# Kernel tuning notes

Hardware: AMD Instinct MI355X
Metric: run time of the kernel (lower is better)

Reference implementation:

```python
import jax, jax.numpy as jnp
import numpy as np


def setup_inputs() -> dict:
    key = jax.random.key(0)
    kq, kk, kv, ki, ks = jax.random.split(key, 5)
    B, H, S, D, VD, T = 2, 8, 2048, 64, 64, 128
    q = jax.random.normal(kq, (B, H, S, D), dtype=jnp.float32)
    k = jax.random.normal(kk, (B, H, S, D), dtype=jnp.float32)
    v = jax.random.normal(kv, (B, H, S, VD), dtype=jnp.float32)
    topk_indices = jax.random.randint(ki, (B, S, T), 0, S, dtype=jnp.int64)
    topk_scores = jax.random.uniform(ks, (B, S, T), dtype=jnp.float32)
    return {"q": q, "k": k, "v": v, "topk_indices": topk_indices,
            "topk_scores": topk_scores}


def reference(q, k, v, topk_indices, topk_scores):
    # q: (B,H,S,D), k: (B,H,S,D), v: (B,H,S,VD), topk_indices: (B,S,T)
    head_dim = q.shape[-1]
    scale = head_dim ** (-0.5)

    # Gather selected K/V per query directly (no O(S^2) expansion).
    # For each batch b: kb (H,S,D), idx (S,T) -> kb[:, idx, :] (H,S,T,D)
    gather = jax.vmap(lambda xb, ib: xb[:, ib, :])
    k_g = gather(k, topk_indices)  # (B,H,S,T,D)
    v_g = gather(v, topk_indices)  # (B,H,S,T,VD)

    # (B,H,S,T) scores
    attn_scores = jnp.einsum('bhsd,bhstd->bhst', q, k_g) * scale
    attn_weights = jax.nn.softmax(attn_scores, axis=-1)

    # reweight by indexer scores (broadcast over heads), then renormalize
    attn_weights = attn_weights * topk_scores[:, None, :, :]
    attn_weights = attn_weights / (attn_weights.sum(axis=-1, keepdims=True) + 1e-12)

    # (B,H,S,VD)
    output = jnp.einsum('bhst,bhstd->bhsd', attn_weights, v_g)
    return output
```

## Files before the change

kernel.cpp:

```cpp
#include <hip/hip_runtime.h>
#include <math.h>


#define BB 2
#define HH 8
#define SS 2048
#define DD 64
#define VDD 64
#define TT 128
#define SCALE 0.125f
#define NKV (BB * HH * SS * DD)

__device__ __forceinline__ float bf_lo(unsigned int u) {
    return __uint_as_float(u << 16);
}
__device__ __forceinline__ float bf_hi(unsigned int u) {
    return __uint_as_float(u);
}
__device__ __forceinline__ unsigned short f2bf_rne(float f) {
    unsigned int u = __float_as_uint(f);
    u += 0x7FFFu + ((u >> 16) & 1u);
    return (unsigned short)(u >> 16);
}

__global__ __launch_bounds__(256) void cvt_kv_bf16(
    const float* __restrict__ k, const float* __restrict__ v,
    unsigned int* __restrict__ kb, unsigned int* __restrict__ vb)
{
    int i = (blockIdx.x * 256 + threadIdx.x) * 4;
    if (i >= NKV) return;
    float4 kf = *(const float4*)(k + i);
    float4 vf = *(const float4*)(v + i);
    unsigned int k0 = (unsigned int)f2bf_rne(kf.x) | ((unsigned int)f2bf_rne(kf.y) << 16);
    unsigned int k1 = (unsigned int)f2bf_rne(kf.z) | ((unsigned int)f2bf_rne(kf.w) << 16);
    unsigned int v0 = (unsigned int)f2bf_rne(vf.x) | ((unsigned int)f2bf_rne(vf.y) << 16);
    unsigned int v1 = (unsigned int)f2bf_rne(vf.z) | ((unsigned int)f2bf_rne(vf.w) << 16);
    *(uint2*)(kb + i / 2) = make_uint2(k0, k1);
    *(uint2*)(vb + i / 2) = make_uint2(v0, v1);
}

__global__ __launch_bounds__(256, 4) void dsa_sparse_attn_bf16(
    const float* __restrict__ q,
    const unsigned int* __restrict__ kb,
    const unsigned int* __restrict__ vb,
    const int* __restrict__ topk_idx,
    const float* __restrict__ topk_sc,
    float* __restrict__ out)
{
    const int tid  = threadIdx.x;
    const int wave = tid >> 6;
    const int lane = tid & 63;
    const int h    = lane & 7;
    const int g    = lane >> 3;

    const int plane = blockIdx.x & 15;
    const int s     = (blockIdx.x >> 4) * 4 + wave;
    const int b     = plane >> 3;

    const float*        qp  = q  + ((size_t)plane * SS + s) * DD;
    const unsigned int* kp  = kb + (size_t)plane * SS * (DD / 2);
    const unsigned int* vp  = vb + (size_t)plane * SS * (VDD / 2);
    const int*          ip  = topk_idx + ((size_t)b * SS + s) * TT;
    const float*        scp = topk_sc  + ((size_t)b * SS + s) * TT;
    float*              op  = out + ((size_t)plane * SS + s) * VDD;

    int   iv0 = ip[lane];
    int   iv1 = ip[64 + lane];
    float sv0 = scp[lane];
    float sv1 = scp[64 + lane];
    float4 qa = *(const float4*)(qp + h * 8);
    float4 qb = *(const float4*)(qp + h * 8 + 4);
    qa.x *= SCALE; qa.y *= SCALE; qa.z *= SCALE; qa.w *= SCALE;
    qb.x *= SCALE; qb.y *= SCALE; qb.z *= SCALE; qb.w *= SCALE;

    float sco[16];
    #pragma unroll
    for (int tc = 0; tc < 8; ++tc) {
        int idx = __shfl(iv0, tc * 8 + g);
        uint4 kk = *(const uint4*)(kp + (size_t)idx * 32 + h * 4);
        float acc;
        acc  = qa.x * bf_lo(kk.x) + qa.y * bf_hi(kk.x);
        acc += qa.z * bf_lo(kk.y) + qa.w * bf_hi(kk.y);
        acc += qb.x * bf_lo(kk.z) + qb.y * bf_hi(kk.z);
        acc += qb.z * bf_lo(kk.w) + qb.w * bf_hi(kk.w);
        acc += __shfl_xor(acc, 1);
        acc += __shfl_xor(acc, 2);
        acc += __shfl_xor(acc, 4);
        sco[tc] = acc;
    }
    #pragma unroll
    for (int tc = 0; tc < 8; ++tc) {
        int idx = __shfl(iv1, tc * 8 + g);
        uint4 kk = *(const uint4*)(kp + (size_t)idx * 32 + h * 4);
        float acc;
        acc  = qa.x * bf_lo(kk.x) + qa.y * bf_hi(kk.x);
        acc += qa.z * bf_lo(kk.y) + qa.w * bf_hi(kk.y);
        acc += qb.x * bf_lo(kk.z) + qb.y * bf_hi(kk.z);
        acc += qb.z * bf_lo(kk.w) + qb.w * bf_hi(kk.w);
        acc += __shfl_xor(acc, 1);
        acc += __shfl_xor(acc, 2);
        acc += __shfl_xor(acc, 4);
        sco[8 + tc] = acc;
    }

    float m = sco[0];
    #pragma unroll
    for (int tc = 1; tc < 16; ++tc) m = fmaxf(m, sco[tc]);
    m = fmaxf(m, __shfl_xor(m, 8));
    m = fmaxf(m, __shfl_xor(m, 16));
    m = fmaxf(m, __shfl_xor(m, 32));
    float sum = 0.f;
    #pragma unroll
    for (int tc = 0; tc < 8; ++tc) {
        float e = __expf(sco[tc] - m) * __shfl(sv0, tc * 8 + g);
        sco[tc] = e;
        sum += e;
    }
    #pragma unroll
    for (int tc = 0; tc < 8; ++tc) {
        float e = __expf(sco[8 + tc] - m) * __shfl(sv1, tc * 8 + g);
        sco[8 + tc] = e;
        sum += e;
    }
    sum += __shfl_xor(sum, 8);
    sum += __shfl_xor(sum, 16);
    sum += __shfl_xor(sum, 32);
    float inv = 1.0f / (sum + 1e-12f);

    float a[8] = {0.f, 0.f, 0.f, 0.f, 0.f, 0.f, 0.f, 0.f};
    #pragma unroll
    for (int tc = 0; tc < 8; ++tc) {
        int   idx = __shfl(iv0, tc * 8 + g);
        float w   = sco[tc] * inv;
        uint4 u = *(const uint4*)(vp + (size_t)idx * 32 + h * 4);
        a[0] = fmaf(w, bf_lo(u.x), a[0]);  a[1] = fmaf(w, bf_hi(u.x), a[1]);
        a[2] = fmaf(w, bf_lo(u.y), a[2]);  a[3] = fmaf(w, bf_hi(u.y), a[3]);
        a[4] = fmaf(w, bf_lo(u.z), a[4]);  a[5] = fmaf(w, bf_hi(u.z), a[5]);
        a[6] = fmaf(w, bf_lo(u.w), a[6]);  a[7] = fmaf(w, bf_hi(u.w), a[7]);
    }
    #pragma unroll
    for (int tc = 0; tc < 8; ++tc) {
        int   idx = __shfl(iv1, tc * 8 + g);
        float w   = sco[8 + tc] * inv;
        uint4 u = *(const uint4*)(vp + (size_t)idx * 32 + h * 4);
        a[0] = fmaf(w, bf_lo(u.x), a[0]);  a[1] = fmaf(w, bf_hi(u.x), a[1]);
        a[2] = fmaf(w, bf_lo(u.y), a[2]);  a[3] = fmaf(w, bf_hi(u.y), a[3]);
        a[4] = fmaf(w, bf_lo(u.z), a[4]);  a[5] = fmaf(w, bf_hi(u.z), a[5]);
        a[6] = fmaf(w, bf_lo(u.w), a[6]);  a[7] = fmaf(w, bf_hi(u.w), a[7]);
    }
    #pragma unroll
    for (int j = 0; j < 8; ++j) {
        a[j] += __shfl_xor(a[j], 8);
        a[j] += __shfl_xor(a[j], 16);
        a[j] += __shfl_xor(a[j], 32);
    }
    if (g == 0) {
        *(float4*)(op + h * 8)     = make_float4(a[0], a[1], a[2], a[3]);
        *(float4*)(op + h * 8 + 4) = make_float4(a[4], a[5], a[6], a[7]);
    }
}

__global__ __launch_bounds__(256, 4) void dsa_sparse_attn_f32(
    const float* __restrict__ q,
    const float* __restrict__ k,
    const float* __restrict__ v,
    const int* __restrict__ topk_idx,
    const float* __restrict__ topk_sc,
    float* __restrict__ out)
{
    const int tid  = threadIdx.x;
    const int wave = tid >> 6;
    const int lane = tid & 63;
    const int plane = blockIdx.x & 15;
    const int s     = (blockIdx.x >> 4) * 4 + wave;
    const int b     = plane >> 3;

    const float* qp  = q + ((size_t)plane * SS + s) * DD;
    const float* kp  = k + (size_t)plane * SS * DD;
    const float* vp  = v + (size_t)plane * SS * VDD;
    const int*   ip  = topk_idx + ((size_t)b * SS + s) * TT;
    const float* scp = topk_sc  + ((size_t)b * SS + s) * TT;
    float*       op  = out + ((size_t)plane * SS + s) * VDD;

    __shared__ int   s_idx[4][TT];
    __shared__ float s_w[4][TT];

    float sc0 = scp[lane];
    float sc1 = scp[64 + lane];
    s_idx[wave][lane]      = ip[lane];
    s_idx[wave][64 + lane] = ip[64 + lane];

    const int l = lane & 3;
    const int g = lane >> 2;
    float4 qf[4];
    #pragma unroll
    for (int j = 0; j < 4; ++j) qf[j] = *(const float4*)(qp + l * 4 + 16 * j);
    __syncthreads();

    #pragma unroll
    for (int tc = 0; tc < 8; ++tc) {
        int t = tc * 16 + g;
        const float* krow = kp + (size_t)s_idx[wave][t] * DD;
        float acc = 0.f;
        #pragma unroll
        for (int j = 0; j < 4; ++j) {
            float4 kf = *(const float4*)(krow + l * 4 + 16 * j);
            acc += qf[j].x * kf.x + qf[j].y * kf.y + qf[j].z * kf.z + qf[j].w * kf.w;
        }
        acc += __shfl_xor(acc, 1);
        acc += __shfl_xor(acc, 2);
        if (l == 0) s_w[wave][t] = acc * SCALE;
    }
    __syncthreads();

    float a0 = s_w[wave][lane];
    float a1 = s_w[wave][64 + lane];
    float m = fmaxf(a0, a1);
    #pragma unroll
    for (int off = 32; off >= 1; off >>= 1) m = fmaxf(m, __shfl_xor(m, off));
    float e0 = __expf(a0 - m) * sc0;
    float e1 = __expf(a1 - m) * sc1;
    float sum = e0 + e1;
    #pragma unroll
    for (int off = 32; off >= 1; off >>= 1) sum += __shfl_xor(sum, off);
    float inv = 1.0f / (sum + 1e-12f);
    s_w[wave][lane]      = e0 * inv;
    s_w[wave][64 + lane] = e1 * inv;
    __syncthreads();

    float acc = 0.f;
    #pragma unroll 8
    for (int t = 0; t < TT; ++t)
        acc = fmaf(s_w[wave][t], vp[(size_t)s_idx[wave][t] * VDD + lane], acc);
    op[lane] = acc;
}

extern "C" void kernel_launch(void* const* d_in, const int* in_sizes, int n_in,
                              void* d_out, int out_size, void* d_ws, size_t ws_size,
                              hipStream_t stream) {
    const float* q   = (const float*)d_in[0];
    const float* k   = (const float*)d_in[1];
    const float* v   = (const float*)d_in[2];
    const int*   idx = (const int*)d_in[3];
    const float* sc  = (const float*)d_in[4];
    float*       out = (float*)d_out;

    const size_t need = (size_t)NKV * 2 * 2;
    if (ws_size >= need) {
        unsigned int* kb = (unsigned int*)d_ws;
        unsigned int* vb = kb + NKV / 2;
        hipLaunchKernelGGL(cvt_kv_bf16, dim3(NKV / 4 / 256), dim3(256), 0, stream,
                           k, v, kb, vb);
        hipLaunchKernelGGL(dsa_sparse_attn_bf16, dim3(8192), dim3(256), 0, stream,
                           q, kb, vb, idx, sc, out);
    } else {
        hipLaunchKernelGGL(dsa_sparse_attn_f32, dim3(8192), dim3(256), 0, stream,
                           q, k, v, idx, sc, out);
    }
}
```

Baseline: 127.1 us.

## Store K as fp16 with dot2 scoring and fuse softmax with V accumulation

K is converted to fp16 (round-toward-zero packing) instead of bf16, so the QK dot products use packed fdot2 instructions rather than unpacking and scalar FMAs. The softmax exponentiation is merged with the V gather/accumulate loop, and normalization is deferred to a single multiply at output time, which removes the second pass over the scores. V accumulation uses 2-wide packed FMAs. This lowers ALU instruction count, but fp16 K has a narrower range and truncating rounding, which changes accuracy.

```diff
diff --git a/kernel.cpp b/kernel.cpp
--- a/kernel.cpp
+++ b/kernel.cpp
@@ -11,6 +11,9 @@
 #define SCALE 0.125f
 #define NKV (BB * HH * SS * DD)
 
+typedef __fp16 h2 __attribute__((ext_vector_type(2)));
+typedef float  f2 __attribute__((ext_vector_type(2)));
+
 __device__ __forceinline__ float bf_lo(unsigned int u) {
     return __uint_as_float(u << 16);
 }
@@ -22,26 +25,34 @@
     u += 0x7FFFu + ((u >> 16) & 1u);
     return (unsigned short)(u >> 16);
 }
-
-__global__ __launch_bounds__(256) void cvt_kv_bf16(
+__device__ __forceinline__ unsigned int pk_f16(float x, float y) {
+    h2 p = __builtin_amdgcn_cvt_pkrtz(x, y);
+    return __builtin_bit_cast(unsigned int, p);
+}
+__device__ __forceinline__ float dot2(unsigned int qh, unsigned int kh, float c) {
+    return __builtin_amdgcn_fdot2(__builtin_bit_cast(h2, qh),
+                                  __builtin_bit_cast(h2, kh), c, false);
+}
+
+__global__ __launch_bounds__(256) void cvt_kv(
     const float* __restrict__ k, const float* __restrict__ v,
-    unsigned int* __restrict__ kb, unsigned int* __restrict__ vb)
+    unsigned int* __restrict__ kh, unsigned int* __restrict__ vb)
 {
     int i = (blockIdx.x * 256 + threadIdx.x) * 4;
     if (i >= NKV) return;
     float4 kf = *(const float4*)(k + i);
     float4 vf = *(const float4*)(v + i);
-    unsigned int k0 = (unsigned int)f2bf_rne(kf.x) | ((unsigned int)f2bf_rne(kf.y) << 16);
-    unsigned int k1 = (unsigned int)f2bf_rne(kf.z) | ((unsigned int)f2bf_rne(kf.w) << 16);
+    unsigned int k0 = pk_f16(kf.x, kf.y);
+    unsigned int k1 = pk_f16(kf.z, kf.w);
     unsigned int v0 = (unsigned int)f2bf_rne(vf.x) | ((unsigned int)f2bf_rne(vf.y) << 16);
     unsigned int v1 = (unsigned int)f2bf_rne(vf.z) | ((unsigned int)f2bf_rne(vf.w) << 16);
-    *(uint2*)(kb + i / 2) = make_uint2(k0, k1);
+    *(uint2*)(kh + i / 2) = make_uint2(k0, k1);
     *(uint2*)(vb + i / 2) = make_uint2(v0, v1);
 }
 
 __global__ __launch_bounds__(256, 4) void dsa_sparse_attn_bf16(
     const float* __restrict__ q,
-    const unsigned int* __restrict__ kb,
+    const unsigned int* __restrict__ kh,
     const unsigned int* __restrict__ vb,
     const int* __restrict__ topk_idx,
     const float* __restrict__ topk_sc,
@@ -58,7 +69,7 @@
     const int b     = plane >> 3;
 
     const float*        qp  = q  + ((size_t)plane * SS + s) * DD;
-    const unsigned int* kp  = kb + (size_t)plane * SS * (DD / 2);
+    const unsigned int* kp  = kh + (size_t)plane * SS * (DD / 2);
     const unsigned int* vp  = vb + (size_t)plane * SS * (VDD / 2);
     const int*          ip  = topk_idx + ((size_t)b * SS + s) * TT;
     const float*        scp = topk_sc  + ((size_t)b * SS + s) * TT;
@@ -70,19 +81,17 @@
     float sv1 = scp[64 + lane];
     float4 qa = *(const float4*)(qp + h * 8);
     float4 qb = *(const float4*)(qp + h * 8 + 4);
-    qa.x *= SCALE; qa.y *= SCALE; qa.z *= SCALE; qa.w *= SCALE;
-    qb.x *= SCALE; qb.y *= SCALE; qb.z *= SCALE; qb.w *= SCALE;
+    unsigned int q0 = pk_f16(qa.x * SCALE, qa.y * SCALE);
+    unsigned int q1 = pk_f16(qa.z * SCALE, qa.w * SCALE);
+    unsigned int q2 = pk_f16(qb.x * SCALE, qb.y * SCALE);
+    unsigned int q3 = pk_f16(qb.z * SCALE, qb.w * SCALE);
 
     float sco[16];
     #pragma unroll
     for (int tc = 0; tc < 8; ++tc) {
         int idx = __shfl(iv0, tc * 8 + g);
         uint4 kk = *(const uint4*)(kp + (size_t)idx * 32 + h * 4);
-        float acc;
-        acc  = qa.x * bf_lo(kk.x) + qa.y * bf_hi(kk.x);
-        acc += qa.z * bf_lo(kk.y) + qa.w * bf_hi(kk.y);
-        acc += qb.x * bf_lo(kk.z) + qb.y * bf_hi(kk.z);
-        acc += qb.z * bf_lo(kk.w) + qb.w * bf_hi(kk.w);
+        float acc = dot2(q0, kk.x, dot2(q1, kk.y, dot2(q2, kk.z, dot2(q3, kk.w, 0.f))));
         acc += __shfl_xor(acc, 1);
         acc += __shfl_xor(acc, 2);
         acc += __shfl_xor(acc, 4);
@@ -92,11 +101,7 @@
     for (int tc = 0; tc < 8; ++tc) {
         int idx = __shfl(iv1, tc * 8 + g);
         uint4 kk = *(const uint4*)(kp + (size_t)idx * 32 + h * 4);
-        float acc;
-        acc  = qa.x * bf_lo(kk.x) + qa.y * bf_hi(kk.x);
-        acc += qa.z * bf_lo(kk.y) + qa.w * bf_hi(kk.y);
-        acc += qb.x * bf_lo(kk.z) + qb.y * bf_hi(kk.z);
-        acc += qb.z * bf_lo(kk.w) + qb.w * bf_hi(kk.w);
+        float acc = dot2(q0, kk.x, dot2(q1, kk.y, dot2(q2, kk.z, dot2(q3, kk.w, 0.f))));
         acc += __shfl_xor(acc, 1);
         acc += __shfl_xor(acc, 2);
         acc += __shfl_xor(acc, 4);
@@ -109,45 +114,47 @@
     m = fmaxf(m, __shfl_xor(m, 8));
     m = fmaxf(m, __shfl_xor(m, 16));
     m = fmaxf(m, __shfl_xor(m, 32));
+
+    f2 a0 = {0.f, 0.f}, a1 = {0.f, 0.f}, a2 = {0.f, 0.f}, a3 = {0.f, 0.f};
     float sum = 0.f;
     #pragma unroll
     for (int tc = 0; tc < 8; ++tc) {
-        float e = __expf(sco[tc] - m) * __shfl(sv0, tc * 8 + g);
-        sco[tc] = e;
+        int   idx = __shfl(iv0, tc * 8 + g);
+        uint4 u   = *(const uint4*)(vp + (size_t)idx * 32 + h * 4);
+        float e   = __expf(sco[tc] - m) * __shfl(sv0, tc * 8 + g);
         sum += e;
-    }
-    #pragma unroll
-    for (int tc = 0; tc < 8; ++tc) {
-        float e = __expf(sco[8 + tc] - m) * __shfl(sv1, tc * 8 + g);
-        sco[8 + tc] = e;
+        f2 wv = {e, e};
+        f2 vx = {bf_lo(u.x), bf_hi(u.x)};
+        f2 vy = {bf_lo(u.y), bf_hi(u.y)};
+        f2 vz = {bf_lo(u.z), bf_hi(u.z)};
+        f2 vw = {bf_lo(u.w), bf_hi(u.w)};
+        a0 = __builtin_elementwise_fma(wv, vx, a0);
+        a1 = __builtin_elementwise_fma(wv, vy, a1);
+        a2 = __builtin_elementwise_fma(wv, vz, a2);
+        a3 = __builtin_elementwise_fma(wv, vw, a3);
+    }
+    #pragma unroll
+    for (int tc = 0; tc < 8; ++tc) {
+        int   idx = __shfl(iv1, tc * 8 + g);
+        uint4 u   = *(const uint4*)(vp + (size_t)idx * 32 + h * 4);
+        float e   = __expf(sco[8 + tc] - m) * __shfl(sv1, tc * 8 + g);
         sum += e;
-    }
+        f2 wv = {e, e};
+        f2 vx = {bf_lo(u.x), bf_hi(u.x)};
+        f2 vy = {bf_lo(u.y), bf_hi(u.y)};
+        f2 vz = {bf_lo(u.z), bf_hi(u.z)};
+        f2 vw = {bf_lo(u.w), bf_hi(u.w)};
+        a0 = __builtin_elementwise_fma(wv, vx, a0);
+        a1 = __builtin_elementwise_fma(wv, vy, a1);
+        a2 = __builtin_elementwise_fma(wv, vz, a2);
+        a3 = __builtin_elementwise_fma(wv, vw, a3);
+    }
+
     sum += __shfl_xor(sum, 8);
     sum += __shfl_xor(sum, 16);
     sum += __shfl_xor(sum, 32);
-    float inv = 1.0f / (sum + 1e-12f);
-
-    float a[8] = {0.f, 0.f, 0.f, 0.f, 0.f, 0.f, 0.f, 0.f};
-    #pragma unroll
-    for (int tc = 0; tc < 8; ++tc) {
-        int   idx = __shfl(iv0, tc * 8 + g);
-        float w   = sco[tc] * inv;
-        uint4 u = *(const uint4*)(vp + (size_t)idx * 32 + h * 4);
-        a[0] = fmaf(w, bf_lo(u.x), a[0]);  a[1] = fmaf(w, bf_hi(u.x), a[1]);
-        a[2] = fmaf(w, bf_lo(u.y), a[2]);  a[3] = fmaf(w, bf_hi(u.y), a[3]);
-        a[4] = fmaf(w, bf_lo(u.z), a[4]);  a[5] = fmaf(w, bf_hi(u.z), a[5]);
-        a[6] = fmaf(w, bf_lo(u.w), a[6]);  a[7] = fmaf(w, bf_hi(u.w), a[7]);
-    }
-    #pragma unroll
-    for (int tc = 0; tc < 8; ++tc) {
-        int   idx = __shfl(iv1, tc * 8 + g);
-        float w   = sco[8 + tc] * inv;
-        uint4 u = *(const uint4*)(vp + (size_t)idx * 32 + h * 4);
-        a[0] = fmaf(w, bf_lo(u.x), a[0]);  a[1] = fmaf(w, bf_hi(u.x), a[1]);
-        a[2] = fmaf(w, bf_lo(u.y), a[2]);  a[3] = fmaf(w, bf_hi(u.y), a[3]);
-        a[4] = fmaf(w, bf_lo(u.z), a[4]);  a[5] = fmaf(w, bf_hi(u.z), a[5]);
-        a[6] = fmaf(w, bf_lo(u.w), a[6]);  a[7] = fmaf(w, bf_hi(u.w), a[7]);
-    }
+
+    float a[8] = {a0.x, a0.y, a1.x, a1.y, a2.x, a2.y, a3.x, a3.y};
     #pragma unroll
     for (int j = 0; j < 8; ++j) {
         a[j] += __shfl_xor(a[j], 8);
@@ -155,8 +162,9 @@
         a[j] += __shfl_xor(a[j], 32);
     }
     if (g == 0) {
-        *(float4*)(op + h * 8)     = make_float4(a[0], a[1], a[2], a[3]);
-        *(float4*)(op + h * 8 + 4) = make_float4(a[4], a[5], a[6], a[7]);
+        float inv = 1.0f / (sum + 1e-12f);
+        *(float4*)(op + h * 8)     = make_float4(a[0] * inv, a[1] * inv, a[2] * inv, a[3] * inv);
+        *(float4*)(op + h * 8 + 4) = make_float4(a[4] * inv, a[5] * inv, a[6] * inv, a[7] * inv);
     }
 }
 
@@ -247,12 +255,12 @@
 
     const size_t need = (size_t)NKV * 2 * 2;
     if (ws_size >= need) {
-        unsigned int* kb = (unsigned int*)d_ws;
-        unsigned int* vb = kb + NKV / 2;
-        hipLaunchKernelGGL(cvt_kv_bf16, dim3(NKV / 4 / 256), dim3(256), 0, stream,
-                           k, v, kb, vb);
+        unsigned int* kh = (unsigned int*)d_ws;
+        unsigned int* vb = kh + NKV / 2;
+        hipLaunchKernelGGL(cvt_kv, dim3(NKV / 4 / 256), dim3(256), 0, stream,
+                           k, v, kh, vb);
         hipLaunchKernelGGL(dsa_sparse_attn_bf16, dim3(8192), dim3(256), 0, stream,
-                           q, kb, vb, idx, sc, out);
+                           q, kh, vb, idx, sc, out);
     } else {
         hipLaunchKernelGGL(dsa_sparse_attn_f32, dim3(8192), dim3(256), 0, stream,
                            q, k, v, idx, sc, out);
```

New measurement: 125.1 us. No clear change (-1.6%).
